# Optimization experiments

Measured on AMD Instinct MI355X. Metric: run time of the kernel, lower is better.

The kernel has to match this reference:

```python
import jax, jax.numpy as jnp
import numpy as np

NEG_BIG = -9e15
ALPHA = 0.2  # leakyrelu slope

N, IN_F, OUT_F = 8192, 512, 64


def setup_inputs() -> dict:
    key = jax.random.key(0)
    ks = jax.random.split(key, 7)
    return {
        "input": jax.random.normal(ks[0], (N, IN_F), dtype=jnp.float32),
        "W": jax.random.normal(ks[1], (IN_F, OUT_F), dtype=jnp.float32) * 0.05,
        "a": jax.random.normal(ks[2], (2 * OUT_F, 1), dtype=jnp.float32) * 0.1,
        "W_si": jax.random.normal(ks[3], (1, 1), dtype=jnp.float32),
        "W_ei": jax.random.normal(ks[4], (1, 1), dtype=jnp.float32),
        "adj_ad": jax.random.uniform(ks[5], (N, N), dtype=jnp.float32),
        "adj": jax.random.randint(ks[6], (N, N), 0, 2, dtype=jnp.int32),
    }


def reference(input, W, a, W_si, W_ei, adj_ad, adj):
    h = input @ W                                   # [N, F]
    F_ = h.shape[1]
    a1, a2 = a[:F_, 0], a[F_:, 0]                   # split concat projection
    # concat-score: a^T [h_i || h_j] == (h@a1)_i + (h@a2)_j, no [N,N,2F] tensor
    e = jax.nn.leaky_relu(h @ a1[:, None] + (h @ a2[:, None]).T, ALPHA)  # [N, N]
    e = jnp.abs(W_ei) * e + jnp.abs(W_si) * adj_ad
    attention = jnp.where(adj > 0, e, jnp.float32(NEG_BIG))
    attention = jax.nn.softmax(attention, axis=1)
    # dropout is identity in eval mode (training=False)
    h_prime = attention @ h                         # [N, F]
    return jax.nn.elu(h_prime)
```

## Files before the change

kernel.cpp:

```cpp
#include <hip/hip_runtime.h>
#include <math.h>

#define N 8192
#define IN_F 512
#define OUTF 64
#define TI 16
#define JSPLIT 4
#define JRANGE (N / JSPLIT)

typedef _Float16 f16x8 __attribute__((ext_vector_type(8)));
typedef float f32x4 __attribute__((ext_vector_type(4)));

typedef const void __attribute__((address_space(1)))* gptr_t;
typedef void __attribute__((address_space(3)))* lptr_t;

#define OFF_HT   0u
#define OFF_S    262144u
#define OFF_T    270336u
#define OFF_TMAX 278528u
#define OFF_SP   278544u
#define OFF_ACC  311312u

__device__ __forceinline__ unsigned enc_f32(float f) {
  unsigned b = __float_as_uint(f);
  return b ^ ((unsigned)((int)b >> 31) | 0x80000000u);
}

__global__ __launch_bounds__(64) void k_precompute(
    const float* __restrict__ input, const float* __restrict__ W,
    const float* __restrict__ a, _Float16* __restrict__ hT,
    float* __restrict__ s, float* __restrict__ t) {
  const int lane = threadIdx.x;
  const int i0 = blockIdx.x * 4;

  float acc[4] = {0.f, 0.f, 0.f, 0.f};
  for (int c = 0; c < IN_F; c += 4) {
    const float w0 = W[(c + 0) * OUTF + lane];
    const float w1 = W[(c + 1) * OUTF + lane];
    const float w2 = W[(c + 2) * OUTF + lane];
    const float w3 = W[(c + 3) * OUTF + lane];
    #pragma unroll
    for (int r = 0; r < 4; r++) {
      const float4 iv = *(const float4*)(input + (size_t)(i0 + r) * IN_F + c);
      acc[r] += iv.x * w0 + iv.y * w1 + iv.z * w2 + iv.w * w3;
    }
  }

  union { _Float16 f[4]; uint2 u; } pk;
  #pragma unroll
  for (int r = 0; r < 4; r++) pk.f[r] = (_Float16)acc[r];
  *(uint2*)(hT + (size_t)lane * N + i0) = pk.u;

  const float a1v = a[lane];
  const float a2v = a[OUTF + lane];
  #pragma unroll
  for (int r = 0; r < 4; r++) {
    float sv = acc[r] * a1v;
    float tv = acc[r] * a2v;
    #pragma unroll
    for (int off = 1; off < 64; off <<= 1) {
      sv += __shfl_xor(sv, off);
      tv += __shfl_xor(tv, off);
    }
    if (lane == 0) {
      s[i0 + r] = sv;
      t[i0 + r] = tv;
    }
  }
}

__global__ __launch_bounds__(512) void k_tmax(const float* __restrict__ t,
                                              unsigned* __restrict__ tmax) {
  __shared__ float red[8];
  const int tid = threadIdx.x;
  float m = t[blockIdx.x * 512 + tid];
  #pragma unroll
  for (int off = 1; off < 64; off <<= 1) m = fmaxf(m, __shfl_xor(m, off));
  if ((tid & 63) == 0) red[tid >> 6] = m;
  __syncthreads();
  if (tid == 0) {
    #pragma unroll
    for (int w = 1; w < 8; w++) m = fmaxf(m, red[w]);
    atomicMax(tmax, enc_f32(m));
  }
}

__global__ __launch_bounds__(64) void k_attn(
    const _Float16* __restrict__ hT, const float* __restrict__ s,
    const float* __restrict__ t, const unsigned* __restrict__ tmaxp,
    const float* __restrict__ W_si, const float* __restrict__ W_ei,
    const float* __restrict__ adj_ad, const int* __restrict__ adj,
    float* __restrict__ SP, float* __restrict__ accP) {
  __shared__ __align__(16) float bufA[2][1024];
  __shared__ __align__(16) int   bufM[2][1024];

  const int lane = threadIdx.x;
  const int q = lane >> 4;
  const int m = lane & 15;
  const int wid = blockIdx.x;
  const int split = wid & (JSPLIT - 1);
  const int i0 = (wid >> 2) * TI;
  const int jb = split * JRANGE;

  const float aei = fabsf(W_ei[0]);
  const float asi = fabsf(W_si[0]);
  const unsigned te = *tmaxp;
  const float tm = __uint_as_float((te & 0x80000000u) ? (te ^ 0x80000000u) : ~te);

  const float sr = s[i0 + m];
  const float xm = sr + tm;
  const float Mr = aei * fmaxf(xm, 0.2f * xm) + asi;

  float S = 0.f;
  f32x4 acc[4];
  #pragma unroll
  for (int nb = 0; nb < 4; nb++) acc[nb] = (f32x4){0.f, 0.f, 0.f, 0.f};

  const size_t stage_ofs = (size_t)(i0 + m) * N + (size_t)(q * 4);

  #define STAGE(b, j0s)                                                        \
    {                                                                          \
      _Pragma("unroll") for (int k = 0; k < 4; k++) {                          \
        __builtin_amdgcn_global_load_lds(                                      \
            (gptr_t)(adj_ad + stage_ofs + (j0s) + k * 16),                     \
            (lptr_t)&bufA[b][k * 256], 16, 0, 0);                              \
      }                                                                        \
      _Pragma("unroll") for (int k = 0; k < 4; k++) {                          \
        __builtin_amdgcn_global_load_lds(                                      \
            (gptr_t)(adj + stage_ofs + (j0s) + k * 16),                        \
            (lptr_t)&bufM[b][k * 256], 16, 0, 0);                              \
      }                                                                        \
    }

  STAGE(0, jb);
  int buf = 0;

  for (int jt = 0; jt < JRANGE; jt += 64) {
    const int j0 = jb + jt;

    if (jt + 64 < JRANGE) {
      STAGE(buf ^ 1, j0 + 64);
      __builtin_amdgcn_s_waitcnt(0xF78);
    } else {
      __builtin_amdgcn_s_waitcnt(0xF70);
    }

    #pragma unroll
    for (int c = 0; c < 2; c++) {
      const int jc0 = c * 8 + q * 2;
      #define LIDX(jc) ((((jc) >> 2) * 256) + (((jc) & 3) * 64) + m * 4)
      const float4 a0 = *(const float4*)&bufA[buf][LIDX(jc0)];
      const float4 a1 = *(const float4*)&bufA[buf][LIDX(jc0 + 1)];
      const int4 k0 = *(const int4*)&bufM[buf][LIDX(jc0)];
      const int4 k1 = *(const int4*)&bufM[buf][LIDX(jc0 + 1)];
      const float4 t0 = *(const float4*)&t[j0 + c * 32 + q * 8];
      const float4 t1 = *(const float4*)&t[j0 + c * 32 + q * 8 + 4];

      const float ad[8] = {a0.x, a0.y, a0.z, a0.w, a1.x, a1.y, a1.z, a1.w};
      const int mk[8] = {k0.x, k0.y, k0.z, k0.w, k1.x, k1.y, k1.z, k1.w};
      const float tv[8] = {t0.x, t0.y, t0.z, t0.w, t1.x, t1.y, t1.z, t1.w};

      f16x8 fa;
      #pragma unroll
      for (int e = 0; e < 8; e++) {
        const float x = sr + tv[e];
        const float ee = aei * fmaxf(x, 0.2f * x) + asi * ad[e];
        const float p = (mk[e] > 0) ? __expf(ee - Mr) : 0.f;
        S += p;
        fa[e] = (_Float16)p;
      }

      #pragma unroll
      for (int nb = 0; nb < 4; nb++) {
        const f16x8 fb = *(const f16x8*)&hT[(size_t)(nb * 16 + m) * N + j0 +
                                            c * 32 + q * 8];
        acc[nb] = __builtin_amdgcn_mfma_f32_16x16x32_f16(fa, fb, acc[nb], 0, 0, 0);
      }
    }
    buf ^= 1;
  }

  S += __shfl_xor(S, 16);
  S += __shfl_xor(S, 32);
  if (lane < 16) SP[(size_t)split * N + i0 + lane] = S;

  #pragma unroll
  for (int nb = 0; nb < 4; nb++) {
    #pragma unroll
    for (int reg = 0; reg < 4; reg++) {
      accP[((size_t)split * N + i0 + q * 4 + reg) * OUTF + nb * 16 + m] =
          acc[nb][reg];
    }
  }
}

__global__ __launch_bounds__(256) void k_combine(const float* __restrict__ accP,
                                                 const float* __restrict__ SP,
                                                 float* __restrict__ out) {
  const int idx = blockIdx.x * 256 + threadIdx.x;
  const int i = idx >> 6;
  float num = 0.f, den = 0.f;
  #pragma unroll
  for (int sp = 0; sp < JSPLIT; sp++) {
    num += accP[(size_t)sp * (N * OUTF) + idx];
    den += SP[(size_t)sp * N + i];
  }
  const float x = num / den;
  out[idx] = x > 0.f ? x : expm1f(x);
}

extern "C" void kernel_launch(void* const* d_in, const int* in_sizes, int n_in,
                              void* d_out, int out_size, void* d_ws, size_t ws_size,
                              hipStream_t stream) {
  const float* input  = (const float*)d_in[0];
  const float* W      = (const float*)d_in[1];
  const float* a      = (const float*)d_in[2];
  const float* W_si   = (const float*)d_in[3];
  const float* W_ei   = (const float*)d_in[4];
  const float* adj_ad = (const float*)d_in[5];
  const int*   adj    = (const int*)d_in[6];
  float* out = (float*)d_out;
  float* ws  = (float*)d_ws;

  _Float16* hT   = (_Float16*)(ws + OFF_HT);
  float* s       = ws + OFF_S;
  float* t       = ws + OFF_T;
  unsigned* tmax = (unsigned*)(ws + OFF_TMAX);
  float* SP      = ws + OFF_SP;
  float* accP    = ws + OFF_ACC;

  hipMemsetAsync(tmax, 0, 4, stream);
  k_precompute<<<N / 4, 64, 0, stream>>>(input, W, a, hT, s, t);
  k_tmax<<<N / 512, 512, 0, stream>>>(t, tmax);
  k_attn<<<(N / TI) * JSPLIT, 64, 0, stream>>>(hT, s, t, tmax, W_si, W_ei,
                                               adj_ad, adj, SP, accP);
  k_combine<<<(N * OUTF) / 256, 256, 0, stream>>>(accP, SP, out);
}
```

Baseline: 619.0 us.

## Replace LDS double-buffered staging with direct loads, double J-split, atomically reduce partials

The attention kernel drops the global_load_lds double-buffer staging of adj_ad and adj and instead reads both matrices straight into registers with vector loads, one tile per loop iteration. The J dimension is split eight ways instead of four to launch more waves. Per-split partial sums are now accumulated with float atomicAdd into one zeroed buffer, which simplifies the combine kernel but adds two memsets and atomic traffic. Without explicit prefetch, memory latency hiding now depends on the extra occupancy, and atomic accumulation makes the summation order nondeterministic.

```diff
diff --git a/kernel.cpp b/kernel.cpp
--- a/kernel.cpp
+++ b/kernel.cpp
@@ -5,21 +5,18 @@
 #define IN_F 512
 #define OUTF 64
 #define TI 16
-#define JSPLIT 4
+#define JSPLIT 8
 #define JRANGE (N / JSPLIT)
 
 typedef _Float16 f16x8 __attribute__((ext_vector_type(8)));
 typedef float f32x4 __attribute__((ext_vector_type(4)));
-
-typedef const void __attribute__((address_space(1)))* gptr_t;
-typedef void __attribute__((address_space(3)))* lptr_t;
 
 #define OFF_HT   0u
 #define OFF_S    262144u
 #define OFF_T    270336u
 #define OFF_TMAX 278528u
 #define OFF_SP   278544u
-#define OFF_ACC  311312u
+#define OFF_ACC  286736u
 
 __device__ __forceinline__ unsigned enc_f32(float f) {
   unsigned b = __float_as_uint(f);
@@ -91,15 +88,12 @@
     const float* __restrict__ W_si, const float* __restrict__ W_ei,
     const float* __restrict__ adj_ad, const int* __restrict__ adj,
     float* __restrict__ SP, float* __restrict__ accP) {
-  __shared__ __align__(16) float bufA[2][1024];
-  __shared__ __align__(16) int   bufM[2][1024];
-
   const int lane = threadIdx.x;
   const int q = lane >> 4;
   const int m = lane & 15;
   const int wid = blockIdx.x;
   const int split = wid & (JSPLIT - 1);
-  const int i0 = (wid >> 2) * TI;
+  const int i0 = (wid >> 3) * TI;
   const int jb = split * JRANGE;
 
   const float aei = fabsf(W_ei[0]);
@@ -116,60 +110,44 @@
   #pragma unroll
   for (int nb = 0; nb < 4; nb++) acc[nb] = (f32x4){0.f, 0.f, 0.f, 0.f};
 
-  const size_t stage_ofs = (size_t)(i0 + m) * N + (size_t)(q * 4);
-
-  #define STAGE(b, j0s)                                                        \
-    {                                                                          \
-      _Pragma("unroll") for (int k = 0; k < 4; k++) {                          \
-        __builtin_amdgcn_global_load_lds(                                      \
-            (gptr_t)(adj_ad + stage_ofs + (j0s) + k * 16),                     \
-            (lptr_t)&bufA[b][k * 256], 16, 0, 0);                              \
-      }                                                                        \
-      _Pragma("unroll") for (int k = 0; k < 4; k++) {                          \
-        __builtin_amdgcn_global_load_lds(                                      \
-            (gptr_t)(adj + stage_ofs + (j0s) + k * 16),                        \
-            (lptr_t)&bufM[b][k * 256], 16, 0, 0);                              \
-      }                                                                        \
-    }
-
-  STAGE(0, jb);
-  int buf = 0;
-
+  const size_t rowA = (size_t)(i0 + m) * N;
+
+  #pragma unroll 1
   for (int jt = 0; jt < JRANGE; jt += 64) {
     const int j0 = jb + jt;
-
-    if (jt + 64 < JRANGE) {
-      STAGE(buf ^ 1, j0 + 64);
-      __builtin_amdgcn_s_waitcnt(0xF78);
-    } else {
-      __builtin_amdgcn_s_waitcnt(0xF70);
-    }
+    const int base = j0 + q * 8;
+
+    const float4 ad0 = *(const float4*)&adj_ad[rowA + base];
+    const float4 ad1 = *(const float4*)&adj_ad[rowA + base + 4];
+    const float4 ad2 = *(const float4*)&adj_ad[rowA + base + 32];
+    const float4 ad3 = *(const float4*)&adj_ad[rowA + base + 36];
+    const int4 mk0 = *(const int4*)&adj[rowA + base];
+    const int4 mk1 = *(const int4*)&adj[rowA + base + 4];
+    const int4 mk2 = *(const int4*)&adj[rowA + base + 32];
+    const int4 mk3 = *(const int4*)&adj[rowA + base + 36];
+    const float4 t0 = *(const float4*)&t[base];
+    const float4 t1 = *(const float4*)&t[base + 4];
+    const float4 t2 = *(const float4*)&t[base + 32];
+    const float4 t3 = *(const float4*)&t[base + 36];
+
+    const float ad[2][8] = {{ad0.x, ad0.y, ad0.z, ad0.w, ad1.x, ad1.y, ad1.z, ad1.w},
+                            {ad2.x, ad2.y, ad2.z, ad2.w, ad3.x, ad3.y, ad3.z, ad3.w}};
+    const int mk[2][8] = {{mk0.x, mk0.y, mk0.z, mk0.w, mk1.x, mk1.y, mk1.z, mk1.w},
+                          {mk2.x, mk2.y, mk2.z, mk2.w, mk3.x, mk3.y, mk3.z, mk3.w}};
+    const float tv[2][8] = {{t0.x, t0.y, t0.z, t0.w, t1.x, t1.y, t1.z, t1.w},
+                            {t2.x, t2.y, t2.z, t2.w, t3.x, t3.y, t3.z, t3.w}};
 
     #pragma unroll
     for (int c = 0; c < 2; c++) {
-      const int jc0 = c * 8 + q * 2;
-      #define LIDX(jc) ((((jc) >> 2) * 256) + (((jc) & 3) * 64) + m * 4)
-      const float4 a0 = *(const float4*)&bufA[buf][LIDX(jc0)];
-      const float4 a1 = *(const float4*)&bufA[buf][LIDX(jc0 + 1)];
-      const int4 k0 = *(const int4*)&bufM[buf][LIDX(jc0)];
-      const int4 k1 = *(const int4*)&bufM[buf][LIDX(jc0 + 1)];
-      const float4 t0 = *(const float4*)&t[j0 + c * 32 + q * 8];
-      const float4 t1 = *(const float4*)&t[j0 + c * 32 + q * 8 + 4];
-
-      const float ad[8] = {a0.x, a0.y, a0.z, a0.w, a1.x, a1.y, a1.z, a1.w};
-      const int mk[8] = {k0.x, k0.y, k0.z, k0.w, k1.x, k1.y, k1.z, k1.w};
-      const float tv[8] = {t0.x, t0.y, t0.z, t0.w, t1.x, t1.y, t1.z, t1.w};
-
       f16x8 fa;
       #pragma unroll
       for (int e = 0; e < 8; e++) {
-        const float x = sr + tv[e];
-        const float ee = aei * fmaxf(x, 0.2f * x) + asi * ad[e];
-        const float p = (mk[e] > 0) ? __expf(ee - Mr) : 0.f;
+        const float x = sr + tv[c][e];
+        const float ee = aei * fmaxf(x, 0.2f * x) + asi * ad[c][e];
+        const float p = (mk[c][e] > 0) ? __expf(ee - Mr) : 0.f;
         S += p;
         fa[e] = (_Float16)p;
       }
-
       #pragma unroll
       for (int nb = 0; nb < 4; nb++) {
         const f16x8 fb = *(const f16x8*)&hT[(size_t)(nb * 16 + m) * N + j0 +
@@ -177,19 +155,18 @@
         acc[nb] = __builtin_amdgcn_mfma_f32_16x16x32_f16(fa, fb, acc[nb], 0, 0, 0);
       }
     }
-    buf ^= 1;
   }
 
   S += __shfl_xor(S, 16);
   S += __shfl_xor(S, 32);
-  if (lane < 16) SP[(size_t)split * N + i0 + lane] = S;
+  if (lane < 16) atomicAdd(&SP[i0 + lane], S);
 
   #pragma unroll
   for (int nb = 0; nb < 4; nb++) {
     #pragma unroll
     for (int reg = 0; reg < 4; reg++) {
-      accP[((size_t)split * N + i0 + q * 4 + reg) * OUTF + nb * 16 + m] =
-          acc[nb][reg];
+      atomicAdd(&accP[(size_t)(i0 + q * 4 + reg) * OUTF + nb * 16 + m],
+                acc[nb][reg]);
     }
   }
 }
@@ -199,13 +176,7 @@
                                                  float* __restrict__ out) {
   const int idx = blockIdx.x * 256 + threadIdx.x;
   const int i = idx >> 6;
-  float num = 0.f, den = 0.f;
-  #pragma unroll
-  for (int sp = 0; sp < JSPLIT; sp++) {
-    num += accP[(size_t)sp * (N * OUTF) + idx];
-    den += SP[(size_t)sp * N + i];
-  }
-  const float x = num / den;
+  const float x = accP[idx] / SP[i];
   out[idx] = x > 0.f ? x : expm1f(x);
 }
 
@@ -230,6 +201,8 @@
   float* accP    = ws + OFF_ACC;
 
   hipMemsetAsync(tmax, 0, 4, stream);
+  hipMemsetAsync(SP, 0, N * sizeof(float), stream);
+  hipMemsetAsync(accP, 0, (size_t)N * OUTF * sizeof(float), stream);
   k_precompute<<<N / 4, 64, 0, stream>>>(input, W, a, hT, s, t);
   k_tmax<<<N / 512, 512, 0, stream>>>(t, tmax);
   k_attn<<<(N / TI) * JSPLIT, 64, 0, stream>>>(hT, s, t, tmax, W_si, W_ei,
```

New measurement: 630.8 us. About the same (+1.9%).

## Double the j-split, reduce partials with atomics, and prefetch hT/t operands

Applied to the files above, without the earlier changes.

The attention kernel now splits each row block's column range 8 ways instead of 4. This doubles the grid of single-wave blocks, and launch bounds are set to request more resident waves per CU, all aimed at hiding the latency of streaming adj_ad and adj. The per-split partial buffers are replaced by float atomicAdd into one zeroed accumulator and one zeroed denominator, which shrinks the workspace and simplifies the combine kernel. The hT and t loads are hoisted ahead of the LDS wait, with scheduling barriers, so they overlap the staged loads. The costs are two extra memsets, atomic contention on the output rows, and a summation order that is no longer deterministic.

```diff
diff --git a/kernel.cpp b/kernel.cpp
--- a/kernel.cpp
+++ b/kernel.cpp
@@ -5,7 +5,7 @@
 #define IN_F 512
 #define OUTF 64
 #define TI 16
-#define JSPLIT 4
+#define JSPLIT 8
 #define JRANGE (N / JSPLIT)
 
 typedef _Float16 f16x8 __attribute__((ext_vector_type(8)));
@@ -19,7 +19,7 @@
 #define OFF_T    270336u
 #define OFF_TMAX 278528u
 #define OFF_SP   278544u
-#define OFF_ACC  311312u
+#define OFF_ACC  286736u
 
 __device__ __forceinline__ unsigned enc_f32(float f) {
   unsigned b = __float_as_uint(f);
@@ -85,7 +85,7 @@
   }
 }
 
-__global__ __launch_bounds__(64) void k_attn(
+__global__ __launch_bounds__(64, 3) void k_attn(
     const _Float16* __restrict__ hT, const float* __restrict__ s,
     const float* __restrict__ t, const unsigned* __restrict__ tmaxp,
     const float* __restrict__ W_si, const float* __restrict__ W_ei,
@@ -99,7 +99,7 @@
   const int m = lane & 15;
   const int wid = blockIdx.x;
   const int split = wid & (JSPLIT - 1);
-  const int i0 = (wid >> 2) * TI;
+  const int i0 = (wid >> 3) * TI;
   const int jb = split * JRANGE;
 
   const float aei = fabsf(W_ei[0]);
@@ -116,19 +116,19 @@
   #pragma unroll
   for (int nb = 0; nb < 4; nb++) acc[nb] = (f32x4){0.f, 0.f, 0.f, 0.f};
 
-  const size_t stage_ofs = (size_t)(i0 + m) * N + (size_t)(q * 4);
+  const size_t rowS = (size_t)(i0 + m) * N + (size_t)(q * 4);
 
   #define STAGE(b, j0s)                                                        \
     {                                                                          \
-      _Pragma("unroll") for (int k = 0; k < 4; k++) {                          \
+      _Pragma("unroll") for (int g = 0; g < 4; g++) {                          \
         __builtin_amdgcn_global_load_lds(                                      \
-            (gptr_t)(adj_ad + stage_ofs + (j0s) + k * 16),                     \
-            (lptr_t)&bufA[b][k * 256], 16, 0, 0);                              \
+            (gptr_t)(adj_ad + rowS + (j0s) + g * 16),                          \
+            (lptr_t)&bufA[b][g * 256], 16, 0, 0);                              \
       }                                                                        \
-      _Pragma("unroll") for (int k = 0; k < 4; k++) {                          \
+      _Pragma("unroll") for (int g = 0; g < 4; g++) {                          \
         __builtin_amdgcn_global_load_lds(                                      \
-            (gptr_t)(adj + stage_ofs + (j0s) + k * 16),                        \
-            (lptr_t)&bufM[b][k * 256], 16, 0, 0);                              \
+            (gptr_t)(adj + rowS + (j0s) + g * 16),                             \
+            (lptr_t)&bufM[b][g * 256], 16, 0, 0);                              \
       }                                                                        \
     }
 
@@ -138,27 +138,41 @@
   for (int jt = 0; jt < JRANGE; jt += 64) {
     const int j0 = jb + jt;
 
+    f16x8 fb[2][4];
+    float4 tf[2][2];
+    #pragma unroll
+    for (int c = 0; c < 2; c++) {
+      tf[c][0] = *(const float4*)&t[j0 + c * 32 + q * 8];
+      tf[c][1] = *(const float4*)&t[j0 + c * 32 + q * 8 + 4];
+      #pragma unroll
+      for (int nb = 0; nb < 4; nb++)
+        fb[c][nb] = *(const f16x8*)&hT[(size_t)(nb * 16 + m) * N + j0 +
+                                       c * 32 + q * 8];
+    }
+    __builtin_amdgcn_sched_barrier(0);
+
     if (jt + 64 < JRANGE) {
       STAGE(buf ^ 1, j0 + 64);
+      __builtin_amdgcn_sched_barrier(0);
       __builtin_amdgcn_s_waitcnt(0xF78);
     } else {
+      __builtin_amdgcn_sched_barrier(0);
       __builtin_amdgcn_s_waitcnt(0xF70);
     }
+    __builtin_amdgcn_sched_barrier(0);
 
     #pragma unroll
     for (int c = 0; c < 2; c++) {
-      const int jc0 = c * 8 + q * 2;
-      #define LIDX(jc) ((((jc) >> 2) * 256) + (((jc) & 3) * 64) + m * 4)
-      const float4 a0 = *(const float4*)&bufA[buf][LIDX(jc0)];
-      const float4 a1 = *(const float4*)&bufA[buf][LIDX(jc0 + 1)];
-      const int4 k0 = *(const int4*)&bufM[buf][LIDX(jc0)];
-      const int4 k1 = *(const int4*)&bufM[buf][LIDX(jc0 + 1)];
-      const float4 t0 = *(const float4*)&t[j0 + c * 32 + q * 8];
-      const float4 t1 = *(const float4*)&t[j0 + c * 32 + q * 8 + 4];
+      const int kc0 = c * 8 + q * 2;
+      const float4 a0 = *(const float4*)&bufA[buf][kc0 * 64 + m * 4];
+      const float4 a1 = *(const float4*)&bufA[buf][(kc0 + 1) * 64 + m * 4];
+      const int4 k0 = *(const int4*)&bufM[buf][kc0 * 64 + m * 4];
+      const int4 k1 = *(const int4*)&bufM[buf][(kc0 + 1) * 64 + m * 4];
 
       const float ad[8] = {a0.x, a0.y, a0.z, a0.w, a1.x, a1.y, a1.z, a1.w};
       const int mk[8] = {k0.x, k0.y, k0.z, k0.w, k1.x, k1.y, k1.z, k1.w};
-      const float tv[8] = {t0.x, t0.y, t0.z, t0.w, t1.x, t1.y, t1.z, t1.w};
+      const float tv[8] = {tf[c][0].x, tf[c][0].y, tf[c][0].z, tf[c][0].w,
+                           tf[c][1].x, tf[c][1].y, tf[c][1].z, tf[c][1].w};
 
       f16x8 fa;
       #pragma unroll
@@ -169,27 +183,24 @@
         S += p;
         fa[e] = (_Float16)p;
       }
-
       #pragma unroll
-      for (int nb = 0; nb < 4; nb++) {
-        const f16x8 fb = *(const f16x8*)&hT[(size_t)(nb * 16 + m) * N + j0 +
-                                            c * 32 + q * 8];
-        acc[nb] = __builtin_amdgcn_mfma_f32_16x16x32_f16(fa, fb, acc[nb], 0, 0, 0);
-      }
+      for (int nb = 0; nb < 4; nb++)
+        acc[nb] = __builtin_amdgcn_mfma_f32_16x16x32_f16(fa, fb[c][nb],
+                                                         acc[nb], 0, 0, 0);
     }
     buf ^= 1;
   }
 
   S += __shfl_xor(S, 16);
   S += __shfl_xor(S, 32);
-  if (lane < 16) SP[(size_t)split * N + i0 + lane] = S;
+  if (lane < 16) atomicAdd(&SP[i0 + lane], S);
 
   #pragma unroll
   for (int nb = 0; nb < 4; nb++) {
     #pragma unroll
     for (int reg = 0; reg < 4; reg++) {
-      accP[((size_t)split * N + i0 + q * 4 + reg) * OUTF + nb * 16 + m] =
-          acc[nb][reg];
+      atomicAdd(&accP[(size_t)(i0 + q * 4 + reg) * OUTF + nb * 16 + m],
+                acc[nb][reg]);
     }
   }
 }
@@ -199,13 +210,7 @@
                                                  float* __restrict__ out) {
   const int idx = blockIdx.x * 256 + threadIdx.x;
   const int i = idx >> 6;
-  float num = 0.f, den = 0.f;
-  #pragma unroll
-  for (int sp = 0; sp < JSPLIT; sp++) {
-    num += accP[(size_t)sp * (N * OUTF) + idx];
-    den += SP[(size_t)sp * N + i];
-  }
-  const float x = num / den;
+  const float x = accP[idx] / SP[i];
   out[idx] = x > 0.f ? x : expm1f(x);
 }
 
@@ -230,6 +235,8 @@
   float* accP    = ws + OFF_ACC;
 
   hipMemsetAsync(tmax, 0, 4, stream);
+  hipMemsetAsync(SP, 0, N * sizeof(float), stream);
+  hipMemsetAsync(accP, 0, (size_t)N * OUTF * sizeof(float), stream);
   k_precompute<<<N / 4, 64, 0, stream>>>(input, W, a, hT, s, t);
   k_tmax<<<N / 512, 512, 0, stream>>>(t, tmax);
   k_attn<<<(N / TI) * JSPLIT, 64, 0, stream>>>(hT, s, t, tmax, W_si, W_ei,
```

After: 625.8 us. About the same (+1.1%).

## Warp-specialize attention kernel with producer waves and fused in-block combine

Applied to the files above, without the earlier changes.

The attention kernel now runs 384-thread blocks over a 16-row tile. Two producer waves stream 256-column tiles of adj_ad and adj into padded, double-buffered LDS. Four consumer waves split the columns and run the exp and MFMA work, then reduce their partials through LDS and apply the normalization and ELU directly. This removes the JSPLIT partial buffers and the separate combine kernel, and uses wide contiguous row loads. In exchange it adds a block barrier per tile, uses more LDS per block (about 66 KB), and launches only 512 blocks.

```diff
diff --git a/kernel.cpp b/kernel.cpp
--- a/kernel.cpp
+++ b/kernel.cpp
@@ -5,8 +5,9 @@
 #define IN_F 512
 #define OUTF 64
 #define TI 16
-#define JSPLIT 4
-#define JRANGE (N / JSPLIT)
+#define JT 256
+#define NTILE (N / JT)
+#define RS 260
 
 typedef _Float16 f16x8 __attribute__((ext_vector_type(8)));
 typedef float f32x4 __attribute__((ext_vector_type(4)));
@@ -18,8 +19,6 @@
 #define OFF_S    262144u
 #define OFF_T    270336u
 #define OFF_TMAX 278528u
-#define OFF_SP   278544u
-#define OFF_ACC  311312u
 
 __device__ __forceinline__ unsigned enc_f32(float f) {
   unsigned b = __float_as_uint(f);
@@ -85,22 +84,21 @@
   }
 }
 
-__global__ __launch_bounds__(64) void k_attn(
+__global__ __launch_bounds__(384, 3) void k_attn(
     const _Float16* __restrict__ hT, const float* __restrict__ s,
     const float* __restrict__ t, const unsigned* __restrict__ tmaxp,
     const float* __restrict__ W_si, const float* __restrict__ W_ei,
     const float* __restrict__ adj_ad, const int* __restrict__ adj,
-    float* __restrict__ SP, float* __restrict__ accP) {
-  __shared__ __align__(16) float bufA[2][1024];
-  __shared__ __align__(16) int   bufM[2][1024];
-
-  const int lane = threadIdx.x;
+    float* __restrict__ out) {
+  __shared__ __align__(16) float bufA[2][TI * RS];
+  __shared__ __align__(16) int   bufM[2][TI * RS];
+
+  const int tid = threadIdx.x;
+  const int wave = tid >> 6;
+  const int lane = tid & 63;
   const int q = lane >> 4;
   const int m = lane & 15;
-  const int wid = blockIdx.x;
-  const int split = wid & (JSPLIT - 1);
-  const int i0 = (wid >> 2) * TI;
-  const int jb = split * JRANGE;
+  const int i0 = blockIdx.x * TI;
 
   const float aei = fabsf(W_ei[0]);
   const float asi = fabsf(W_si[0]);
@@ -116,97 +114,104 @@
   #pragma unroll
   for (int nb = 0; nb < 4; nb++) acc[nb] = (f32x4){0.f, 0.f, 0.f, 0.f};
 
-  const size_t stage_ofs = (size_t)(i0 + m) * N + (size_t)(q * 4);
+  const int p = wave - 4;
 
   #define STAGE(b, j0s)                                                        \
     {                                                                          \
-      _Pragma("unroll") for (int k = 0; k < 4; k++) {                          \
+      _Pragma("unroll") for (int g = 0; g < 8; g++) {                          \
+        const int row = p * 8 + g;                                             \
         __builtin_amdgcn_global_load_lds(                                      \
-            (gptr_t)(adj_ad + stage_ofs + (j0s) + k * 16),                     \
-            (lptr_t)&bufA[b][k * 256], 16, 0, 0);                              \
+            (gptr_t)(adj_ad + (size_t)(i0 + row) * N + (j0s) + lane * 4),      \
+            (lptr_t)&bufA[b][row * RS], 16, 0, 0);                             \
       }                                                                        \
-      _Pragma("unroll") for (int k = 0; k < 4; k++) {                          \
+      _Pragma("unroll") for (int g = 0; g < 8; g++) {                          \
+        const int row = p * 8 + g;                                             \
         __builtin_amdgcn_global_load_lds(                                      \
-            (gptr_t)(adj + stage_ofs + (j0s) + k * 16),                        \
-            (lptr_t)&bufM[b][k * 256], 16, 0, 0);                              \
+            (gptr_t)(adj + (size_t)(i0 + row) * N + (j0s) + lane * 4),         \
+            (lptr_t)&bufM[b][row * RS], 16, 0, 0);                             \
       }                                                                        \
     }
 
-  STAGE(0, jb);
-  int buf = 0;
-
-  for (int jt = 0; jt < JRANGE; jt += 64) {
-    const int j0 = jb + jt;
-
-    if (jt + 64 < JRANGE) {
-      STAGE(buf ^ 1, j0 + 64);
-      __builtin_amdgcn_s_waitcnt(0xF78);
+  if (wave >= 4) STAGE(0, 0);
+
+  #pragma unroll 1
+  for (int k = 0; k < NTILE; k++) {
+    __syncthreads();
+
+    if (wave >= 4) {
+      if (k + 1 < NTILE) STAGE((k + 1) & 1, (k + 1) * JT);
     } else {
-      __builtin_amdgcn_s_waitcnt(0xF70);
-    }
-
-    #pragma unroll
-    for (int c = 0; c < 2; c++) {
-      const int jc0 = c * 8 + q * 2;
-      #define LIDX(jc) ((((jc) >> 2) * 256) + (((jc) & 3) * 64) + m * 4)
-      const float4 a0 = *(const float4*)&bufA[buf][LIDX(jc0)];
-      const float4 a1 = *(const float4*)&bufA[buf][LIDX(jc0 + 1)];
-      const int4 k0 = *(const int4*)&bufM[buf][LIDX(jc0)];
-      const int4 k1 = *(const int4*)&bufM[buf][LIDX(jc0 + 1)];
-      const float4 t0 = *(const float4*)&t[j0 + c * 32 + q * 8];
-      const float4 t1 = *(const float4*)&t[j0 + c * 32 + q * 8 + 4];
-
-      const float ad[8] = {a0.x, a0.y, a0.z, a0.w, a1.x, a1.y, a1.z, a1.w};
-      const int mk[8] = {k0.x, k0.y, k0.z, k0.w, k1.x, k1.y, k1.z, k1.w};
-      const float tv[8] = {t0.x, t0.y, t0.z, t0.w, t1.x, t1.y, t1.z, t1.w};
-
-      f16x8 fa;
+      const int buf = k & 1;
+      const int j0 = k * JT;
       #pragma unroll
-      for (int e = 0; e < 8; e++) {
-        const float x = sr + tv[e];
-        const float ee = aei * fmaxf(x, 0.2f * x) + asi * ad[e];
-        const float p = (mk[e] > 0) ? __expf(ee - Mr) : 0.f;
-        S += p;
-        fa[e] = (_Float16)p;
+      for (int ck = 0; ck < 2; ck++) {
+        const int kc = 2 * wave + ck;
+        const int cb = j0 + kc * 32 + q * 8;
+        const int lb = m * RS + kc * 32 + q * 8;
+
+        const float4 tfa = *(const float4*)&t[cb];
+        const float4 tfb = *(const float4*)&t[cb + 4];
+        const float4 a0 = *(const float4*)&bufA[buf][lb];
+        const float4 a1 = *(const float4*)&bufA[buf][lb + 4];
+        const int4 k0 = *(const int4*)&bufM[buf][lb];
+        const int4 k1 = *(const int4*)&bufM[buf][lb + 4];
+
+        const float ad[8] = {a0.x, a0.y, a0.z, a0.w, a1.x, a1.y, a1.z, a1.w};
+        const int mk[8] = {k0.x, k0.y, k0.z, k0.w, k1.x, k1.y, k1.z, k1.w};
+        const float tv[8] = {tfa.x, tfa.y, tfa.z, tfa.w,
+                             tfb.x, tfb.y, tfb.z, tfb.w};
+
+        f16x8 fa;
+        #pragma unroll
+        for (int e = 0; e < 8; e++) {
+          const float x = sr + tv[e];
+          const float ee = aei * fmaxf(x, 0.2f * x) + asi * ad[e];
+          const float pv = (mk[e] > 0) ? __expf(ee - Mr) : 0.f;
+          S += pv;
+          fa[e] = (_Float16)pv;
+        }
+        #pragma unroll
+        for (int nb = 0; nb < 4; nb++) {
+          const f16x8 fb = *(const f16x8*)&hT[(size_t)(nb * 16 + m) * N + cb];
+          acc[nb] = __builtin_amdgcn_mfma_f32_16x16x32_f16(fa, fb, acc[nb],
+                                                           0, 0, 0);
+        }
       }
-
+    }
+  }
+
+  float* aLDS = &bufA[0][0];
+  float* sLDS = (float*)&bufM[0][0];
+
+  if (wave < 4) {
+    sLDS[wave * 64 + lane] = S;
+    #pragma unroll
+    for (int nb = 0; nb < 4; nb++) {
       #pragma unroll
-      for (int nb = 0; nb < 4; nb++) {
-        const f16x8 fb = *(const f16x8*)&hT[(size_t)(nb * 16 + m) * N + j0 +
-                                            c * 32 + q * 8];
-        acc[nb] = __builtin_amdgcn_mfma_f32_16x16x32_f16(fa, fb, acc[nb], 0, 0, 0);
+      for (int reg = 0; reg < 4; reg++) {
+        aLDS[wave * 1024 + (q * 4 + reg) * 64 + nb * 16 + m] = acc[nb][reg];
       }
     }
-    buf ^= 1;
-  }
-
-  S += __shfl_xor(S, 16);
-  S += __shfl_xor(S, 32);
-  if (lane < 16) SP[(size_t)split * N + i0 + lane] = S;
-
-  #pragma unroll
-  for (int nb = 0; nb < 4; nb++) {
-    #pragma unroll
-    for (int reg = 0; reg < 4; reg++) {
-      accP[((size_t)split * N + i0 + q * 4 + reg) * OUTF + nb * 16 + m] =
-          acc[nb][reg];
-    }
-  }
-}
-
-__global__ __launch_bounds__(256) void k_combine(const float* __restrict__ accP,
-                                                 const float* __restrict__ SP,
-                                                 float* __restrict__ out) {
-  const int idx = blockIdx.x * 256 + threadIdx.x;
-  const int i = idx >> 6;
-  float num = 0.f, den = 0.f;
-  #pragma unroll
-  for (int sp = 0; sp < JSPLIT; sp++) {
-    num += accP[(size_t)sp * (N * OUTF) + idx];
-    den += SP[(size_t)sp * N + i];
-  }
-  const float x = num / den;
-  out[idx] = x > 0.f ? x : expm1f(x);
+  }
+  __syncthreads();
+
+  if (wave < 4) {
+    #pragma unroll
+    for (int ii = 0; ii < 4; ii++) {
+      const int e = tid + 256 * ii;
+      const int r = e >> 6;
+      const int f = e & 63;
+      float num = 0.f, den = 0.f;
+      #pragma unroll
+      for (int w = 0; w < 4; w++) {
+        num += aLDS[w * 1024 + r * 64 + f];
+        #pragma unroll
+        for (int qq = 0; qq < 4; qq++) den += sLDS[w * 64 + qq * 16 + r];
+      }
+      const float x = num / den;
+      out[(size_t)(i0 + r) * OUTF + f] = x > 0.f ? x : expm1f(x);
+    }
+  }
 }
 
 extern "C" void kernel_launch(void* const* d_in, const int* in_sizes, int n_in,
@@ -226,13 +231,10 @@
   float* s       = ws + OFF_S;
   float* t       = ws + OFF_T;
   unsigned* tmax = (unsigned*)(ws + OFF_TMAX);
-  float* SP      = ws + OFF_SP;
-  float* accP    = ws + OFF_ACC;
 
   hipMemsetAsync(tmax, 0, 4, stream);
   k_precompute<<<N / 4, 64, 0, stream>>>(input, W, a, hT, s, t);
   k_tmax<<<N / 512, 512, 0, stream>>>(t, tmax);
-  k_attn<<<(N / TI) * JSPLIT, 64, 0, stream>>>(hT, s, t, tmax, W_si, W_ei,
-                                               adj_ad, adj, SP, accP);
-  k_combine<<<(N * OUTF) / 256, 256, 0, stream>>>(accP, SP, out);
-}
+  k_attn<<<N / TI, 384, 0, stream>>>(hT, s, t, tmax, W_si, W_ei,
+                                     adj_ad, adj, out);
+}
```

Result: faster. 583.8 us (-5.7%).
